# Kernel tuning notes

Hardware: AMD Instinct MI355X
Metric: run time of the kernel (lower is better)

The kernel has to match this reference:

```python
import jax, jax.numpy as jnp
import numpy as np

B, T, D = 128, 512, 400
N_VALS, N_ACTS = 1024, 128

def setup_inputs() -> dict:
    key = jax.random.key(0)
    ks = jax.random.split(key, 7)
    H_utt = jax.random.normal(ks[0], (B, T, D), dtype=jnp.float32)
    c_utt = jax.random.normal(ks[1], (B, D), dtype=jnp.float32)
    C_acts = jax.random.normal(ks[2], (B, N_ACTS, D), dtype=jnp.float32)
    C_vals = jax.random.normal(ks[3], (N_VALS, 1, D), dtype=jnp.float32)
    W_score = jax.random.normal(ks[4], (1, D), dtype=jnp.float32) * (1.0 / np.sqrt(D))
    b_score = jnp.zeros((1,), dtype=jnp.float32)
    lens = jax.random.randint(ks[5], (B,), T // 2, T + 1, dtype=jnp.int64 if jax.config.read('jax_enable_x64') else jnp.int32)
    lens = lens.at[0].set(T)  # ensure max(lens) == T so masking matches torch semantics
    return {"H_utt": H_utt, "c_utt": c_utt, "C_acts": C_acts, "C_vals": C_vals,
            "W_score": W_score, "b_score": b_score, "utterance_len": lens}

def reference(H_utt, c_utt, C_acts, C_vals, W_score, b_score, utterance_len):
    vals = C_vals[:, 0, :]                                   # [V, D]
    # --- y_utts: default attention of each value vector over utterance states ---
    scores = jnp.einsum('btd,vd->bvt', H_utt, vals)          # mul+sum scoring
    mask = jnp.arange(T)[None, :] < utterance_len[:, None]   # [B, T]
    scores = jnp.where(mask[:, None, :], scores, -jnp.inf)
    probs = jax.nn.softmax(scores, axis=-1)                  # [B, V, T]
    q_utts = jnp.einsum('bvt,btd->bvd', probs, H_utt)        # weighted sum contexts
    y_utts = jnp.einsum('bvd,d->bv', q_utts, W_score[0]) + b_score[0]  # utt_scorer
    # --- y_acts: attention of c_utt over per-example act vectors, then score vs vals ---
    s2 = jnp.einsum('bad,bd->ba', C_acts, c_utt)
    p2 = jax.nn.softmax(s2, axis=-1)
    q_acts = jnp.einsum('ba,bad->bd', p2, C_acts)            # [B, D]
    y_acts = q_acts @ vals.T                                 # [B, V]
    return (y_utts, y_acts)
```

## Files before the change

kernel.cpp:

```cpp
#include <hip/hip_runtime.h>
#include <hip/hip_bf16.h>

#define B_  128
#define T_  512
#define D_  400
#define NV  1024
#define NA  128

#define LDH   416
#define NT    32
#define TILEB (NT * LDH * 2)
#define CHUNKS_PER_TILE (TILEB/16)
#define MV    128

typedef __bf16 bf16_t;
typedef bf16_t bf16x8 __attribute__((ext_vector_type(8)));
typedef float  floatx4 __attribute__((ext_vector_type(4)));

__device__ inline void async_copy16(const void* g, void* l) {
    __builtin_amdgcn_global_load_lds(
        (const __attribute__((address_space(1))) unsigned int*)g,
        (__attribute__((address_space(3))) unsigned int*)l, 16, 0, 0);
}

__device__ inline float dot4(float4 a, float4 b) {
    return a.x * b.x + a.y * b.y + a.z * b.z + a.w * b.w;
}

template<int PRE>
__global__ __launch_bounds__(256) void prep_kernel(const float* __restrict__ H,
                                                   const float* __restrict__ W,
                                                   const float* __restrict__ cu,
                                                   const float* __restrict__ Ca,
                                                   float* __restrict__ hw,
                                                   bf16_t* __restrict__ Hbf,
                                                   float* __restrict__ q_ws) {
    __shared__ __align__(16) float4 cu4[100];
    __shared__ float s_lds[NA];
    __shared__ float p_lds[NA];
    __shared__ float red[8];
    __shared__ __align__(16) float4 part[100];

    int tid = threadIdx.x, wave = tid >> 6, lane = tid & 63;

    if (blockIdx.x < (B_ * T_ / 4)) {
        long row = (long)blockIdx.x * 4 + wave;
        int key = (int)(row & 7);
        const float* h = H + row * D_;
        float acc = 0.f;
        if (lane < 50) {
            const float4* p  = (const float4*)(h + lane * 8);
            const float4* wp = (const float4*)(W + lane * 8);
            float4 x = p[0], y = p[1];
            acc = dot4(x, wp[0]) + dot4(y, wp[1]);
            if (PRE) {
                bf16x8 f;
                f[0] = (bf16_t)x.x; f[1] = (bf16_t)x.y; f[2] = (bf16_t)x.z; f[3] = (bf16_t)x.w;
                f[4] = (bf16_t)y.x; f[5] = (bf16_t)y.y; f[6] = (bf16_t)y.z; f[7] = (bf16_t)y.w;
                int pos = (lane < 48) ? (lane ^ key) : lane;
                *(bf16x8*)(Hbf + row * (long)LDH + pos * 8) = f;
            }
        } else if (PRE && lane < 52) {
            bf16x8 z;
#pragma unroll
            for (int j = 0; j < 8; ++j) z[j] = (bf16_t)0.0f;
            *(bf16x8*)(Hbf + row * (long)LDH + lane * 8) = z;
        }
#pragma unroll
        for (int off = 1; off < 64; off <<= 1) acc += __shfl_xor(acc, off, 64);
        if (lane == 0) hw[row] = acc;
        return;
    }

    int b = blockIdx.x - (B_ * T_ / 4);

    if (tid < 100) cu4[tid] = ((const float4*)(cu + (size_t)b * D_))[tid];
    __syncthreads();

    const float4* Cb4 = (const float4*)(Ca + (size_t)b * NA * D_);
#pragma unroll 2
    for (int i = 0; i < 32; ++i) {
        int a = wave * 32 + i;
        const float4* row = Cb4 + (size_t)a * 100;
        float acc = dot4(row[lane], cu4[lane]);
        if (lane < 36) acc += dot4(row[lane + 64], cu4[lane + 64]);
#pragma unroll
        for (int off = 1; off < 64; off <<= 1) acc += __shfl_xor(acc, off, 64);
        if (lane == 0) s_lds[a] = acc;
    }
    __syncthreads();

    float s = (tid < NA) ? s_lds[tid] : -3.0e38f;
    float m = s;
#pragma unroll
    for (int off = 1; off < 64; off <<= 1) m = fmaxf(m, __shfl_xor(m, off, 64));
    if (lane == 0) red[wave] = m;
    __syncthreads();
    m = fmaxf(red[0], red[1]);
    float e = (tid < NA) ? __expf(s - m) : 0.f;
    float sum = e;
#pragma unroll
    for (int off = 1; off < 64; off <<= 1) sum += __shfl_xor(sum, off, 64);
    if (lane == 0) red[4 + wave] = sum;
    __syncthreads();
    float S = red[4] + red[5];
    if (tid < NA) p_lds[tid] = e / S;
    __syncthreads();

    int c4 = tid % 100;
    int half = tid / 100;
    float4 acc0 = {0.f, 0.f, 0.f, 0.f};
    if (tid < 200) {
        float4 acc1 = {0.f, 0.f, 0.f, 0.f};
        int a0 = half * 64;
#pragma unroll 4
        for (int a = 0; a < 64; a += 2) {
            float p0 = p_lds[a0 + a], p1 = p_lds[a0 + a + 1];
            float4 x0 = Cb4[(size_t)(a0 + a) * 100 + c4];
            float4 x1 = Cb4[(size_t)(a0 + a + 1) * 100 + c4];
            acc0.x += p0 * x0.x; acc0.y += p0 * x0.y; acc0.z += p0 * x0.z; acc0.w += p0 * x0.w;
            acc1.x += p1 * x1.x; acc1.y += p1 * x1.y; acc1.z += p1 * x1.z; acc1.w += p1 * x1.w;
        }
        acc0.x += acc1.x; acc0.y += acc1.y; acc0.z += acc1.z; acc0.w += acc1.w;
        if (half == 1) part[c4] = acc0;
    }
    __syncthreads();
    if (tid < 100) {
        float4 o = part[c4];
        o.x += acc0.x; o.y += acc0.y; o.z += acc0.z; o.w += acc0.w;
        ((float4*)(q_ws + (size_t)b * D_))[c4] = o;
    }
}

template<int PRE>
__global__ __launch_bounds__(256, 2) void main_kernel(const float* __restrict__ H,
                                                      const bf16_t* __restrict__ Hbf,
                                                      const float* __restrict__ Cv,
                                                      const float* __restrict__ hw,
                                                      const float* __restrict__ q_ws,
                                                      const float* __restrict__ bs,
                                                      const int* __restrict__ lens,
                                                      float* __restrict__ out) {
    __shared__ __align__(16) char lds_raw[3 * TILEB + 2048];
    char* Lbuf = lds_raw;
    float* hw_f = (float*)(lds_raw + 3 * TILEB);

    int i = blockIdx.x;
    int xcd = i & 7, vc = (i >> 3) & 7, bb = i >> 6;
    int b = xcd + 8 * bb;
    int vbase = vc * MV;

    int tid = threadIdx.x;
    int wave = tid >> 6, lane = tid & 63;
    int lrow = lane & 15, quad = lane >> 4;

    int len = lens[b];
    float b0 = bs[0];
    int ntiles = (len + NT - 1) / NT;

    const float* Hb = H + (size_t)b * T_ * D_;
    const bf16_t* Hbfb = Hbf + (size_t)b * T_ * LDH;
    const float* hwb = hw + (size_t)b * T_;

    bf16x8 afrag[2][13];
#pragma unroll
    for (int set = 0; set < 2; ++set) {
        const float* vrow = Cv + (size_t)(vbase + wave * 32 + set * 16 + lrow) * D_;
#pragma unroll
        for (int kk = 0; kk < 13; ++kk) {
            int k0 = kk * 32 + quad * 8;
            bf16x8 f;
            if (k0 >= D_) {
#pragma unroll
                for (int j = 0; j < 8; ++j) f[j] = (bf16_t)0.0f;
            } else {
                const float4* p = (const float4*)(vrow + k0);
                float4 x = p[0], y = p[1];
                f[0] = (bf16_t)x.x; f[1] = (bf16_t)x.y;
                f[2] = (bf16_t)x.z; f[3] = (bf16_t)x.w;
                f[4] = (bf16_t)y.x; f[5] = (bf16_t)y.y;
                f[6] = (bf16_t)y.z; f[7] = (bf16_t)y.w;
            }
            afrag[set][kk] = f;
        }
    }

    float m_s[2][4], l_s[2][4], a_s[2][4];
#pragma unroll
    for (int set = 0; set < 2; ++set)
#pragma unroll
        for (int r = 0; r < 4; ++r) { m_s[set][r] = -3.0e38f; l_s[set][r] = 0.f; a_s[set][r] = 0.f; }

    auto stage = [&](int loff, int tt) {
        const char* gt = (const char*)(Hbfb + (size_t)tt * NT * LDH);
        char* lt = Lbuf + loff;
        int cbase = wave * 416 + lane;
#pragma unroll
        for (int k = 0; k < 7; ++k) {
            int c = cbase + (k << 6);
            if (lane + (k << 6) < 416)
                async_copy16(gt + c * 16, lt + c * 16);
        }
    };

    auto stage_f32 = [&](int loff, int tt) {
        for (int idx = tid; idx < NT * 50; idx += 256) {
            int r = idx / 50, c = idx - r * 50;
            const float4* s = (const float4*)(Hb + (size_t)(tt * NT + r) * D_ + c * 8);
            float4 x = s[0], y = s[1];
            bf16x8 f;
            f[0] = (bf16_t)x.x; f[1] = (bf16_t)x.y; f[2] = (bf16_t)x.z; f[3] = (bf16_t)x.w;
            f[4] = (bf16_t)y.x; f[5] = (bf16_t)y.y; f[6] = (bf16_t)y.z; f[7] = (bf16_t)y.w;
            int pos = (c < 48) ? (c ^ (r & 7)) : c;
            *(bf16x8*)(Lbuf + loff + r * 832 + pos * 16) = f;
        }
    };

    int o0 = 0, o1 = TILEB, o2 = 2 * TILEB;

    if (PRE) {
        if (tid < 128) async_copy16((const char*)hwb + tid * 16, (char*)hw_f + tid * 16);
        asm volatile("s_waitcnt vmcnt(0)" ::: "memory");
        stage(o0, 0);
        stage(o1, 1);
        __builtin_amdgcn_s_barrier();
    } else {
        if (tid < 256) ((float2*)hw_f)[tid] = ((const float2*)hwb)[tid];
        for (int idx = tid; idx < 3 * NT * 2; idx += 256) {
            int bu = idx / (NT * 2), rem = idx % (NT * 2);
            int r = rem >> 1, c = 50 + (rem & 1);
            bf16x8 z;
#pragma unroll
            for (int j = 0; j < 8; ++j) z[j] = (bf16_t)0.0f;
            *(bf16x8*)(Lbuf + bu * TILEB + r * 832 + c * 16) = z;
        }
        __syncthreads();
    }

    const int swz = (lrow & 7) << 4;
    const int rowb0 = lrow * 832;
    const int rowb1 = (16 + lrow) * 832;

    for (int tt = 0; tt < ntiles; ++tt) {
        if (PRE) {
            asm volatile("s_waitcnt lgkmcnt(0)" ::: "memory");
            __builtin_amdgcn_s_barrier();
            if (tt + 2 < ntiles) {
                stage(o2, tt + 2);
                asm volatile("s_waitcnt vmcnt(14)" ::: "memory");
            } else if (tt + 1 < ntiles) {
                asm volatile("s_waitcnt vmcnt(7)" ::: "memory");
            } else {
                asm volatile("s_waitcnt vmcnt(0)" ::: "memory");
            }
            __builtin_amdgcn_sched_barrier(0);
        } else {
            __syncthreads();
            stage_f32(o0, tt);
            __syncthreads();
        }

        int t0 = tt * NT;
        float hwv[2];
#pragma unroll
        for (int s = 0; s < 2; ++s) hwv[s] = hw_f[t0 + s * 16 + lrow];

        floatx4 c[2][2];
        floatx4 zero4 = {0.f, 0.f, 0.f, 0.f};
#pragma unroll
        for (int set = 0; set < 2; ++set)
#pragma unroll
            for (int s = 0; s < 2; ++s) c[set][s] = zero4;

        const char* L = (const char*)(Lbuf + o0);
#pragma unroll
        for (int kk = 0; kk < 13; ++kk) {
            int koffb = kk * 64 + quad * 16;
            int o = (kk < 12) ? (koffb ^ swz) : koffb;
            bf16x8 f0 = *(const bf16x8*)(L + rowb0 + o);
            c[0][0] = __builtin_amdgcn_mfma_f32_16x16x32_bf16(afrag[0][kk], f0, c[0][0], 0, 0, 0);
            c[1][0] = __builtin_amdgcn_mfma_f32_16x16x32_bf16(afrag[1][kk], f0, c[1][0], 0, 0, 0);
            bf16x8 f1 = *(const bf16x8*)(L + rowb1 + o);
            c[0][1] = __builtin_amdgcn_mfma_f32_16x16x32_bf16(afrag[0][kk], f1, c[0][1], 0, 0, 0);
            c[1][1] = __builtin_amdgcn_mfma_f32_16x16x32_bf16(afrag[1][kk], f1, c[1][1], 0, 0, 0);
        }

        if (t0 + NT > len) {
#pragma unroll
            for (int s = 0; s < 2; ++s) {
                int t = t0 + s * 16 + lrow;
                if (t >= len) {
#pragma unroll
                    for (int set = 0; set < 2; ++set) {
                        c[set][s][0] = -3.0e38f; c[set][s][1] = -3.0e38f;
                        c[set][s][2] = -3.0e38f; c[set][s][3] = -3.0e38f;
                    }
                }
            }
        }

#pragma unroll
        for (int set = 0; set < 2; ++set)
#pragma unroll
            for (int r = 0; r < 4; ++r) {
                float cm = fmaxf(c[set][0][r], c[set][1][r]);
                float mn = fmaxf(m_s[set][r], cm);
                float alpha = __expf(m_s[set][r] - mn);
                float ps = 0.f, qs = 0.f;
#pragma unroll
                for (int s = 0; s < 2; ++s) {
                    float p = __expf(c[set][s][r] - mn);
                    ps += p;
                    qs += p * hwv[s];
                }
                l_s[set][r] = l_s[set][r] * alpha + ps;
                a_s[set][r] = a_s[set][r] * alpha + qs;
                m_s[set][r] = mn;
            }

        int tmp = o0; o0 = o1; o1 = o2; o2 = tmp;
    }

#pragma unroll
    for (int set = 0; set < 2; ++set)
#pragma unroll
        for (int r = 0; r < 4; ++r) {
            float m = m_s[set][r], l = l_s[set][r], a = a_s[set][r];
#pragma unroll
            for (int off = 1; off < 16; off <<= 1) {
                float mo = __shfl_xor(m, off, 64);
                float lo = __shfl_xor(l, off, 64);
                float ao = __shfl_xor(a, off, 64);
                float mn = fmaxf(m, mo);
                float f1 = __expf(m - mn), f2 = __expf(mo - mn);
                l = l * f1 + lo * f2;
                a = a * f1 + ao * f2;
                m = mn;
            }
            if (lrow == 0) {
                int v = vbase + wave * 32 + set * 16 + quad * 4 + r;
                out[(size_t)b * NV + v] = a / l + b0;
            }
        }

    {
        const float4* q4 = (const float4*)(q_ws + (size_t)b * D_);
        float4 qa = q4[lane];
        float4 qb = (lane < 36) ? q4[lane + 64] : make_float4(0.f, 0.f, 0.f, 0.f);
#pragma unroll 1
        for (int ii = 0; ii < 32; ii += 4) {
            int v0 = vbase + wave * 32 + ii;
            float acc[4];
#pragma unroll
            for (int r = 0; r < 4; ++r) {
                const float4* v4 = (const float4*)(Cv + (size_t)(v0 + r) * D_);
                acc[r] = dot4(v4[lane], qa);
                if (lane < 36) acc[r] += dot4(v4[lane + 64], qb);
            }
#pragma unroll
            for (int off = 1; off < 64; off <<= 1) {
#pragma unroll
                for (int r = 0; r < 4; ++r) acc[r] += __shfl_xor(acc[r], off, 64);
            }
            if (lane == 0) {
                float4 o = make_float4(acc[0], acc[1], acc[2], acc[3]);
                *(float4*)(out + (size_t)B_ * NV + (size_t)b * NV + v0) = o;
            }
        }
    }
}

extern "C" void kernel_launch(void* const* d_in, const int* in_sizes, int n_in,
                              void* d_out, int out_size, void* d_ws, size_t ws_size,
                              hipStream_t stream) {
    const float* H    = (const float*)d_in[0];
    const float* cu   = (const float*)d_in[1];
    const float* Ca   = (const float*)d_in[2];
    const float* Cv   = (const float*)d_in[3];
    const float* W    = (const float*)d_in[4];
    const float* bs   = (const float*)d_in[5];
    const int*   lens = (const int*)d_in[6];
    float* out = (float*)d_out;

    float*  hw   = (float*)d_ws;
    float*  q_ws = hw + (size_t)B_ * T_;
    bf16_t* Hbf  = (bf16_t*)(q_ws + (size_t)B_ * D_);

    size_t need = ((size_t)B_ * T_ + (size_t)B_ * D_) * sizeof(float)
                + (size_t)B_ * T_ * LDH * sizeof(bf16_t);
    bool pre = (ws_size >= need);

    dim3 pgrid(B_ * T_ / 4 + B_);
    if (pre) {
        prep_kernel<1><<<pgrid, dim3(256), 0, stream>>>(H, W, cu, Ca, hw, Hbf, q_ws);
        main_kernel<1><<<dim3(1024), dim3(256), 0, stream>>>(H, Hbf, Cv, hw, q_ws, bs, lens, out);
    } else {
        prep_kernel<0><<<pgrid, dim3(256), 0, stream>>>(H, W, cu, Ca, hw, Hbf, q_ws);
        main_kernel<0><<<dim3(1024), dim3(256), 0, stream>>>(H, Hbf, Cv, hw, q_ws, bs, lens, out);
    }
}
```

Baseline: 312.1 us.

## Drop bf16 pre-conversion of H; stage fp32 tiles directly with double buffering

Removes the prep pass that wrote a padded, swizzled bf16 copy of H. The main kernel now loads fp32 H tiles and converts them to bf16 in LDS using a two-buffer prefetch, in place of the async global-to-LDS triple buffer. The y_acts GEMV moves from the main kernel into the per-batch blocks of the prep kernel. Softmax switches to exp2 by folding log2e into the value fragments, and the MFMA section is wrapped in s_setprio. This avoids writing and re-reading a ~54MB bf16 workspace, but each main-kernel block now converts fp32 H on the fly, and the 8 blocks sharing a batch each read the fp32 rows.

```diff
diff --git a/kernel.cpp b/kernel.cpp
--- a/kernel.cpp
+++ b/kernel.cpp
@@ -10,31 +10,24 @@
 #define LDH   416
 #define NT    32
 #define TILEB (NT * LDH * 2)
-#define CHUNKS_PER_TILE (TILEB/16)
 #define MV    128
+#define LOG2E 1.4426950408889634f
 
 typedef __bf16 bf16_t;
 typedef bf16_t bf16x8 __attribute__((ext_vector_type(8)));
 typedef float  floatx4 __attribute__((ext_vector_type(4)));
 
-__device__ inline void async_copy16(const void* g, void* l) {
-    __builtin_amdgcn_global_load_lds(
-        (const __attribute__((address_space(1))) unsigned int*)g,
-        (__attribute__((address_space(3))) unsigned int*)l, 16, 0, 0);
-}
-
 __device__ inline float dot4(float4 a, float4 b) {
     return a.x * b.x + a.y * b.y + a.z * b.z + a.w * b.w;
 }
 
-template<int PRE>
 __global__ __launch_bounds__(256) void prep_kernel(const float* __restrict__ H,
                                                    const float* __restrict__ W,
                                                    const float* __restrict__ cu,
                                                    const float* __restrict__ Ca,
+                                                   const float* __restrict__ Cv,
                                                    float* __restrict__ hw,
-                                                   bf16_t* __restrict__ Hbf,
-                                                   float* __restrict__ q_ws) {
+                                                   float* __restrict__ out) {
     __shared__ __align__(16) float4 cu4[100];
     __shared__ float s_lds[NA];
     __shared__ float p_lds[NA];
@@ -43,28 +36,14 @@
 
     int tid = threadIdx.x, wave = tid >> 6, lane = tid & 63;
 
-    if (blockIdx.x < (B_ * T_ / 4)) {
-        long row = (long)blockIdx.x * 4 + wave;
-        int key = (int)(row & 7);
+    if (blockIdx.x >= B_) {
+        long row = (long)(blockIdx.x - B_) * 4 + wave;
         const float* h = H + row * D_;
         float acc = 0.f;
         if (lane < 50) {
             const float4* p  = (const float4*)(h + lane * 8);
             const float4* wp = (const float4*)(W + lane * 8);
-            float4 x = p[0], y = p[1];
-            acc = dot4(x, wp[0]) + dot4(y, wp[1]);
-            if (PRE) {
-                bf16x8 f;
-                f[0] = (bf16_t)x.x; f[1] = (bf16_t)x.y; f[2] = (bf16_t)x.z; f[3] = (bf16_t)x.w;
-                f[4] = (bf16_t)y.x; f[5] = (bf16_t)y.y; f[6] = (bf16_t)y.z; f[7] = (bf16_t)y.w;
-                int pos = (lane < 48) ? (lane ^ key) : lane;
-                *(bf16x8*)(Hbf + row * (long)LDH + pos * 8) = f;
-            }
-        } else if (PRE && lane < 52) {
-            bf16x8 z;
-#pragma unroll
-            for (int j = 0; j < 8; ++j) z[j] = (bf16_t)0.0f;
-            *(bf16x8*)(Hbf + row * (long)LDH + lane * 8) = z;
+            acc = dot4(p[0], wp[0]) + dot4(p[1], wp[1]);
         }
 #pragma unroll
         for (int off = 1; off < 64; off <<= 1) acc += __shfl_xor(acc, off, 64);
@@ -72,7 +51,7 @@
         return;
     }
 
-    int b = blockIdx.x - (B_ * T_ / 4);
+    int b = blockIdx.x;
 
     if (tid < 100) cu4[tid] = ((const float4*)(cu + (size_t)b * D_))[tid];
     __syncthreads();
@@ -128,27 +107,49 @@
     if (tid < 100) {
         float4 o = part[c4];
         o.x += acc0.x; o.y += acc0.y; o.z += acc0.z; o.w += acc0.w;
-        ((float4*)(q_ws + (size_t)b * D_))[c4] = o;
+        cu4[c4] = o;
+    }
+    __syncthreads();
+
+    {
+        float4 qa = cu4[lane];
+        float4 qb = (lane < 36) ? cu4[lane + 64] : make_float4(0.f, 0.f, 0.f, 0.f);
+#pragma unroll 2
+        for (int g = 0; g < 64; ++g) {
+            int v0 = wave * 256 + g * 4;
+            float acc[4];
+#pragma unroll
+            for (int r = 0; r < 4; ++r) {
+                const float4* v4 = (const float4*)(Cv + (size_t)(v0 + r) * D_);
+                acc[r] = dot4(v4[lane], qa);
+                if (lane < 36) acc[r] += dot4(v4[lane + 64], qb);
+            }
+#pragma unroll
+            for (int off = 1; off < 64; off <<= 1) {
+#pragma unroll
+                for (int r = 0; r < 4; ++r) acc[r] += __shfl_xor(acc[r], off, 64);
+            }
+            if (lane == 0) {
+                float4 o = make_float4(acc[0], acc[1], acc[2], acc[3]);
+                *(float4*)(out + (size_t)B_ * NV + (size_t)b * NV + v0) = o;
+            }
+        }
     }
 }
 
-template<int PRE>
 __global__ __launch_bounds__(256, 2) void main_kernel(const float* __restrict__ H,
-                                                      const bf16_t* __restrict__ Hbf,
                                                       const float* __restrict__ Cv,
                                                       const float* __restrict__ hw,
-                                                      const float* __restrict__ q_ws,
                                                       const float* __restrict__ bs,
                                                       const int* __restrict__ lens,
                                                       float* __restrict__ out) {
-    __shared__ __align__(16) char lds_raw[3 * TILEB + 2048];
+    __shared__ __align__(16) char lds_raw[2 * TILEB + 2048];
     char* Lbuf = lds_raw;
-    float* hw_f = (float*)(lds_raw + 3 * TILEB);
+    float* hw_f = (float*)(lds_raw + 2 * TILEB);
 
     int i = blockIdx.x;
-    int xcd = i & 7, vc = (i >> 3) & 7, bb = i >> 6;
-    int b = xcd + 8 * bb;
-    int vbase = vc * MV;
+    int b = (i & 7) + 8 * (i >> 6);
+    int vbase = ((i >> 3) & 7) * MV;
 
     int tid = threadIdx.x;
     int wave = tid >> 6, lane = tid & 63;
@@ -159,8 +160,6 @@
     int ntiles = (len + NT - 1) / NT;
 
     const float* Hb = H + (size_t)b * T_ * D_;
-    const bf16_t* Hbfb = Hbf + (size_t)b * T_ * LDH;
-    const float* hwb = hw + (size_t)b * T_;
 
     bf16x8 afrag[2][13];
 #pragma unroll
@@ -176,10 +175,10 @@
             } else {
                 const float4* p = (const float4*)(vrow + k0);
                 float4 x = p[0], y = p[1];
-                f[0] = (bf16_t)x.x; f[1] = (bf16_t)x.y;
-                f[2] = (bf16_t)x.z; f[3] = (bf16_t)x.w;
-                f[4] = (bf16_t)y.x; f[5] = (bf16_t)y.y;
-                f[6] = (bf16_t)y.z; f[7] = (bf16_t)y.w;
+                f[0] = (bf16_t)(x.x * LOG2E); f[1] = (bf16_t)(x.y * LOG2E);
+                f[2] = (bf16_t)(x.z * LOG2E); f[3] = (bf16_t)(x.w * LOG2E);
+                f[4] = (bf16_t)(y.x * LOG2E); f[5] = (bf16_t)(y.y * LOG2E);
+                f[6] = (bf16_t)(y.z * LOG2E); f[7] = (bf16_t)(y.w * LOG2E);
             }
             afrag[set][kk] = f;
         }
@@ -190,18 +189,6 @@
     for (int set = 0; set < 2; ++set)
 #pragma unroll
         for (int r = 0; r < 4; ++r) { m_s[set][r] = -3.0e38f; l_s[set][r] = 0.f; a_s[set][r] = 0.f; }
-
-    auto stage = [&](int loff, int tt) {
-        const char* gt = (const char*)(Hbfb + (size_t)tt * NT * LDH);
-        char* lt = Lbuf + loff;
-        int cbase = wave * 416 + lane;
-#pragma unroll
-        for (int k = 0; k < 7; ++k) {
-            int c = cbase + (k << 6);
-            if (lane + (k << 6) < 416)
-                async_copy16(gt + c * 16, lt + c * 16);
-        }
-    };
 
     auto stage_f32 = [&](int loff, int tt) {
         for (int idx = tid; idx < NT * 50; idx += 256) {
@@ -216,49 +203,25 @@
         }
     };
 
-    int o0 = 0, o1 = TILEB, o2 = 2 * TILEB;
-
-    if (PRE) {
-        if (tid < 128) async_copy16((const char*)hwb + tid * 16, (char*)hw_f + tid * 16);
-        asm volatile("s_waitcnt vmcnt(0)" ::: "memory");
-        stage(o0, 0);
-        stage(o1, 1);
-        __builtin_amdgcn_s_barrier();
-    } else {
-        if (tid < 256) ((float2*)hw_f)[tid] = ((const float2*)hwb)[tid];
-        for (int idx = tid; idx < 3 * NT * 2; idx += 256) {
-            int bu = idx / (NT * 2), rem = idx % (NT * 2);
-            int r = rem >> 1, c = 50 + (rem & 1);
-            bf16x8 z;
-#pragma unroll
-            for (int j = 0; j < 8; ++j) z[j] = (bf16_t)0.0f;
-            *(bf16x8*)(Lbuf + bu * TILEB + r * 832 + c * 16) = z;
-        }
-        __syncthreads();
-    }
+    ((float2*)hw_f)[tid] = ((const float2*)(hw + (size_t)b * T_))[tid];
+    if (tid < 128) {
+        int bu = tid >> 6, rem = tid & 63;
+        int r = rem >> 1, c = 50 + (rem & 1);
+        bf16x8 z;
+#pragma unroll
+        for (int j = 0; j < 8; ++j) z[j] = (bf16_t)0.0f;
+        *(bf16x8*)(Lbuf + bu * TILEB + r * 832 + c * 16) = z;
+    }
+    stage_f32(0, 0);
+    __syncthreads();
 
     const int swz = (lrow & 7) << 4;
     const int rowb0 = lrow * 832;
     const int rowb1 = (16 + lrow) * 832;
 
     for (int tt = 0; tt < ntiles; ++tt) {
-        if (PRE) {
-            asm volatile("s_waitcnt lgkmcnt(0)" ::: "memory");
-            __builtin_amdgcn_s_barrier();
-            if (tt + 2 < ntiles) {
-                stage(o2, tt + 2);
-                asm volatile("s_waitcnt vmcnt(14)" ::: "memory");
-            } else if (tt + 1 < ntiles) {
-                asm volatile("s_waitcnt vmcnt(7)" ::: "memory");
-            } else {
-                asm volatile("s_waitcnt vmcnt(0)" ::: "memory");
-            }
-            __builtin_amdgcn_sched_barrier(0);
-        } else {
-            __syncthreads();
-            stage_f32(o0, tt);
-            __syncthreads();
-        }
+        int cur = tt & 1;
+        if (tt + 1 < ntiles) stage_f32((cur ^ 1) * TILEB, tt + 1);
 
         int t0 = tt * NT;
         float hwv[2];
@@ -272,7 +235,8 @@
 #pragma unroll
             for (int s = 0; s < 2; ++s) c[set][s] = zero4;
 
-        const char* L = (const char*)(Lbuf + o0);
+        const char* L = (const char*)(Lbuf + cur * TILEB);
+        __builtin_amdgcn_s_setprio(1);
 #pragma unroll
         for (int kk = 0; kk < 13; ++kk) {
             int koffb = kk * 64 + quad * 16;
@@ -284,6 +248,7 @@
             c[0][1] = __builtin_amdgcn_mfma_f32_16x16x32_bf16(afrag[0][kk], f1, c[0][1], 0, 0, 0);
             c[1][1] = __builtin_amdgcn_mfma_f32_16x16x32_bf16(afrag[1][kk], f1, c[1][1], 0, 0, 0);
         }
+        __builtin_amdgcn_s_setprio(0);
 
         if (t0 + NT > len) {
 #pragma unroll
@@ -305,11 +270,11 @@
             for (int r = 0; r < 4; ++r) {
                 float cm = fmaxf(c[set][0][r], c[set][1][r]);
                 float mn = fmaxf(m_s[set][r], cm);
-                float alpha = __expf(m_s[set][r] - mn);
+                float alpha = __builtin_amdgcn_exp2f(m_s[set][r] - mn);
                 float ps = 0.f, qs = 0.f;
 #pragma unroll
                 for (int s = 0; s < 2; ++s) {
-                    float p = __expf(c[set][s][r] - mn);
+                    float p = __builtin_amdgcn_exp2f(c[set][s][r] - mn);
                     ps += p;
                     qs += p * hwv[s];
                 }
@@ -318,7 +283,7 @@
                 m_s[set][r] = mn;
             }
 
-        int tmp = o0; o0 = o1; o1 = o2; o2 = tmp;
+        __syncthreads();
     }
 
 #pragma unroll
@@ -332,7 +297,8 @@
                 float lo = __shfl_xor(l, off, 64);
                 float ao = __shfl_xor(a, off, 64);
                 float mn = fmaxf(m, mo);
-                float f1 = __expf(m - mn), f2 = __expf(mo - mn);
+                float f1 = __builtin_amdgcn_exp2f(m - mn);
+                float f2 = __builtin_amdgcn_exp2f(mo - mn);
                 l = l * f1 + lo * f2;
                 a = a * f1 + ao * f2;
                 m = mn;
@@ -342,32 +308,6 @@
                 out[(size_t)b * NV + v] = a / l + b0;
             }
         }
-
-    {
-        const float4* q4 = (const float4*)(q_ws + (size_t)b * D_);
-        float4 qa = q4[lane];
-        float4 qb = (lane < 36) ? q4[lane + 64] : make_float4(0.f, 0.f, 0.f, 0.f);
-#pragma unroll 1
-        for (int ii = 0; ii < 32; ii += 4) {
-            int v0 = vbase + wave * 32 + ii;
-            float acc[4];
-#pragma unroll
-            for (int r = 0; r < 4; ++r) {
-                const float4* v4 = (const float4*)(Cv + (size_t)(v0 + r) * D_);
-                acc[r] = dot4(v4[lane], qa);
-                if (lane < 36) acc[r] += dot4(v4[lane + 64], qb);
-            }
-#pragma unroll
-            for (int off = 1; off < 64; off <<= 1) {
-#pragma unroll
-                for (int r = 0; r < 4; ++r) acc[r] += __shfl_xor(acc[r], off, 64);
-            }
-            if (lane == 0) {
-                float4 o = make_float4(acc[0], acc[1], acc[2], acc[3]);
-                *(float4*)(out + (size_t)B_ * NV + (size_t)b * NV + v0) = o;
-            }
-        }
-    }
 }
 
 extern "C" void kernel_launch(void* const* d_in, const int* in_sizes, int n_in,
@@ -382,20 +322,8 @@
     const int*   lens = (const int*)d_in[6];
     float* out = (float*)d_out;
 
-    float*  hw   = (float*)d_ws;
-    float*  q_ws = hw + (size_t)B_ * T_;
-    bf16_t* Hbf  = (bf16_t*)(q_ws + (size_t)B_ * D_);
-
-    size_t need = ((size_t)B_ * T_ + (size_t)B_ * D_) * sizeof(float)
-                + (size_t)B_ * T_ * LDH * sizeof(bf16_t);
-    bool pre = (ws_size >= need);
-
-    dim3 pgrid(B_ * T_ / 4 + B_);
-    if (pre) {
-        prep_kernel<1><<<pgrid, dim3(256), 0, stream>>>(H, W, cu, Ca, hw, Hbf, q_ws);
-        main_kernel<1><<<dim3(1024), dim3(256), 0, stream>>>(H, Hbf, Cv, hw, q_ws, bs, lens, out);
-    } else {
-        prep_kernel<0><<<pgrid, dim3(256), 0, stream>>>(H, W, cu, Ca, hw, Hbf, q_ws);
-        main_kernel<0><<<dim3(1024), dim3(256), 0, stream>>>(H, Hbf, Cv, hw, q_ws, bs, lens, out);
-    }
+    float* hw = (float*)d_ws;
+
+    prep_kernel<<<dim3(B_ + B_ * T_ / 4), dim3(256), 0, stream>>>(H, W, cu, Ca, Cv, hw, out);
+    main_kernel<<<dim3(1024), dim3(256), 0, stream>>>(H, Cv, hw, bs, lens, out);
 }
```

Measured after the change: 529.5 us. 69.7% more time.
